# Kernel tuning notes

Hardware: AMD Instinct MI355X
Metric: run time of the kernel (lower is better)

Reference implementation:

```python
import jax, jax.numpy as jnp
import numpy as np

T, B, D, H = 1024, 4, 1024, 16
HD = D // H  # 64


def _layernorm(x, g, b, eps=1e-5):
    mu = jnp.mean(x, axis=-1, keepdims=True)
    var = jnp.var(x, axis=-1, keepdims=True)
    return (x - mu) / jnp.sqrt(var + eps) * g + b


def setup_inputs() -> dict:
    key = jax.random.key(0)
    ks = jax.random.split(key, 16)
    s = 1.0 / np.sqrt(D)
    mk = lambda k: jax.random.uniform(k, (D, D), jnp.float32, -s, s)
    return {
        "x": jax.random.normal(ks[0], (T, B, D), jnp.float32),
        "Wq": mk(ks[1]), "bq": jnp.zeros((D,), jnp.float32),
        "Wk": mk(ks[2]), "bk": jnp.zeros((D,), jnp.float32),
        "Wv": mk(ks[3]), "bv": jnp.zeros((D,), jnp.float32),
        "Wo": mk(ks[4]), "bo": jnp.zeros((D,), jnp.float32),
        "Wl": mk(ks[5]), "bl": jnp.zeros((D,), jnp.float32),
        "g1": jnp.ones((D,), jnp.float32), "b1": jnp.zeros((D,), jnp.float32),
        "g2": jnp.ones((D,), jnp.float32), "b2": jnp.zeros((D,), jnp.float32),
    }


def reference(x, Wq, bq, Wk, bk, Wv, bv, Wo, bo, Wl, bl, g1, b1, g2, b2):
    # x: [T, B, D] (time-major). The torch loop over dim 0 with full keys/values
    # is equivalent to batched full (non-causal) self-attention.
    q = (x @ Wq.T + bq).reshape(T, B, H, HD)
    k = (x @ Wk.T + bk).reshape(T, B, H, HD)
    v = (x @ Wv.T + bv).reshape(T, B, H, HD)
    scores = jnp.einsum("tbhd,sbhd->bhts", q, k) / np.sqrt(HD).astype(np.float32)
    attn = jax.nn.softmax(scores, axis=-1)          # [B,H,T,T]
    ctx = jnp.einsum("bhts,sbhd->tbhd", attn, v).reshape(T, B, D)
    attn_out = ctx @ Wo.T + bo
    # dropout p: identity at inference
    h = _layernorm(attn_out + x, g1, b1)
    ffn = h @ Wl.T + bl
    return _layernorm(ffn + h, g2, b2)
```

## Files before the change

kernel.cpp:

```cpp
#include <hip/hip_runtime.h>

#define T_ 1024
#define B_ 4
#define D_ 1024
#define H_ 16
#define HD_ 64
#define M_ (T_ * B_)

typedef _Float16 f16;
typedef f16 f16x8 __attribute__((ext_vector_type(8)));
typedef f16 f16x4 __attribute__((ext_vector_type(4)));
typedef float f32x4 __attribute__((ext_vector_type(4)));

__device__ __forceinline__ void gl2lds16(const void* g, void* l) {
  __builtin_amdgcn_global_load_lds(
      (const __attribute__((address_space(1))) void*)g,
      (__attribute__((address_space(3))) void*)l, 16, 0, 0);
}

__global__ __launch_bounds__(256) void cvt_f32_f16(const float* __restrict__ in,
                                                   f16* __restrict__ out, int n) {
  int i = (blockIdx.x * 256 + threadIdx.x) * 4;
  if (i >= n) return;
  float4 v = *(const float4*)(in + i);
  f16x4 o = {(f16)v.x, (f16)v.y, (f16)v.z, (f16)v.w};
  *(f16x4*)(out + i) = o;
}

struct WPtrs {
  const float* s[5];
  f16* d[5];
};

__global__ __launch_bounds__(256) void cvt5(WPtrs p) {
  const int a = blockIdx.x >> 10;
  const int i = ((blockIdx.x & 1023) * 256 + threadIdx.x) * 4;
  float4 v = *(const float4*)(p.s[a] + i);
  f16x4 o = {(f16)v.x, (f16)v.y, (f16)v.z, (f16)v.w};
  *(f16x4*)(p.d[a] + i) = o;
}

__global__ __launch_bounds__(256) void bcat(const float* __restrict__ b0,
                                            const float* __restrict__ b1,
                                            const float* __restrict__ b2,
                                            float* __restrict__ dst) {
  const float* src = blockIdx.x == 0 ? b0 : (blockIdx.x == 1 ? b1 : b2);
  const int i = threadIdx.x * 4;
  *(float4*)(dst + blockIdx.x * 1024 + i) = *(const float4*)(src + i);
}

__global__ __launch_bounds__(256) void gemm_f16(const f16* __restrict__ A,
                                                const f16* __restrict__ W,
                                                const float* __restrict__ bias,
                                                float* __restrict__ out) {
  constexpr int K = D_, BK = 32;
  __shared__ __align__(16) f16 As[128 * BK];
  __shared__ __align__(16) f16 Bs[64 * BK];
  const int tid = threadIdx.x;
  const int lane = tid & 63;
  const int quad = lane >> 4, l16 = lane & 15;
  const int m0 = blockIdx.y * 128, n0 = blockIdx.x * 64;
  const int wave = tid >> 6;
  const int wm = (wave >> 1) * 64, wn = (wave & 1) * 32;
  f32x4 acc[4][2] = {};
  for (int kt = 0; kt < K / BK; ++kt) {
    __syncthreads();
    const int kb = kt * BK;
#pragma unroll
    for (int i = 0; i < 2; ++i) {
      const int c = i * 256 + tid;
      const int row = c >> 2, col8 = (c & 3) * 8;
      const int ldsbase = (i * 256 + (tid & ~63)) * 8;
      gl2lds16(A + (size_t)(m0 + row) * K + kb + col8, &As[ldsbase]);
    }
    {
      const int row = tid >> 2, col8 = (tid & 3) * 8;
      const int ldsbase = (tid & ~63) * 8;
      gl2lds16(W + (size_t)(n0 + row) * K + kb + col8, &Bs[ldsbase]);
    }
    __syncthreads();
    f16x8 af[4], bf[2];
#pragma unroll
    for (int i = 0; i < 4; ++i)
      af[i] = *(const f16x8*)&As[(wm + i * 16 + l16) * BK + quad * 8];
#pragma unroll
    for (int j = 0; j < 2; ++j)
      bf[j] = *(const f16x8*)&Bs[(wn + j * 16 + l16) * BK + quad * 8];
#pragma unroll
    for (int i = 0; i < 4; ++i)
#pragma unroll
      for (int j = 0; j < 2; ++j)
        acc[i][j] = __builtin_amdgcn_mfma_f32_16x16x32_f16(af[i], bf[j], acc[i][j], 0, 0, 0);
  }
#pragma unroll
  for (int j = 0; j < 2; ++j) {
    const int n = n0 + wn + j * 16 + l16;
    const float bn = bias[n];
#pragma unroll
    for (int i = 0; i < 4; ++i) {
      const int m = m0 + wm + i * 16 + quad * 4;
#pragma unroll
      for (int r = 0; r < 4; ++r)
        out[(size_t)(m + r) * D_ + n] = acc[i][j][r] + bn;
    }
  }
}

#define QSCALE 0.18033688011112042f
__global__ __launch_bounds__(256) void gemm_qkv(const f16* __restrict__ A,
                                                const f16* __restrict__ W,
                                                const float* __restrict__ bias,
                                                f16* __restrict__ qo,
                                                f16* __restrict__ ko,
                                                f16* __restrict__ vo) {
  constexpr int K = D_, BK = 32;
  __shared__ __align__(16) f16 As[128 * BK];
  __shared__ __align__(16) f16 Bs[128 * BK];
  const int tid = threadIdx.x;
  const int lane = tid & 63;
  const int quad = lane >> 4, l16 = lane & 15;
  const int m0 = blockIdx.y * 128, n0 = blockIdx.x * 128;
  const int wave = tid >> 6;
  const int wm = (wave >> 1) * 64, wn = (wave & 1) * 64;
  f32x4 acc[4][4] = {};
  for (int kt = 0; kt < K / BK; ++kt) {
    __syncthreads();
    const int kb = kt * BK;
#pragma unroll
    for (int i = 0; i < 2; ++i) {
      const int c = i * 256 + tid;
      const int row = c >> 2, col8 = (c & 3) * 8;
      const int ldsbase = (i * 256 + (tid & ~63)) * 8;
      gl2lds16(A + (size_t)(m0 + row) * K + kb + col8, &As[ldsbase]);
      gl2lds16(W + (size_t)(n0 + row) * K + kb + col8, &Bs[ldsbase]);
    }
    __syncthreads();
    f16x8 af[4], bf[4];
#pragma unroll
    for (int i = 0; i < 4; ++i)
      af[i] = *(const f16x8*)&As[(wm + i * 16 + l16) * BK + quad * 8];
#pragma unroll
    for (int j = 0; j < 4; ++j)
      bf[j] = *(const f16x8*)&Bs[(wn + j * 16 + l16) * BK + quad * 8];
#pragma unroll
    for (int i = 0; i < 4; ++i)
#pragma unroll
      for (int j = 0; j < 4; ++j)
        acc[i][j] = __builtin_amdgcn_mfma_f32_16x16x32_f16(af[i], bf[j], acc[i][j], 0, 0, 0);
  }
  const int which = n0 >> 10;
  f16* outp = which == 0 ? qo : (which == 1 ? ko : vo);
  const float sc = which == 0 ? QSCALE : 1.0f;
#pragma unroll
  for (int j = 0; j < 4; ++j) {
    const int n = n0 + wn + j * 16 + l16;
    const float bn = bias[n];
    const int nl = n & 1023;
    const int hh = nl >> 6, d = nl & 63;
#pragma unroll
    for (int i = 0; i < 4; ++i) {
#pragma unroll
      for (int r = 0; r < 4; ++r) {
        const int m = m0 + wm + i * 16 + quad * 4 + r;
        const float v = (acc[i][j][r] + bn) * sc;
        const int t = m >> 2, bb = m & 3;
        if (which < 2)
          outp[((size_t)(bb * H_ + hh) * T_ + t) * HD_ + d] = (f16)v;
        else
          outp[((size_t)(bb * H_ + hh) * HD_ + d) * T_ + t] = (f16)v;
      }
    }
  }
}

__global__ __launch_bounds__(256) void attn(const f16* __restrict__ Q,
                                            const f16* __restrict__ Km,
                                            const f16* __restrict__ Vt,
                                            f16* __restrict__ ctx) {
  constexpr int SK = 128;
  constexpr int NT = T_ / SK;
  __shared__ __align__(16) f16 Ks[SK * HD_];
  __shared__ __align__(16) f16 Vs[HD_ * SK];
  __shared__ __align__(16) f16 Ps[4][16 * 36];
  const int tid = threadIdx.x, wave = tid >> 6, lane = tid & 63;
  const int quad = lane >> 4, l16 = lane & 15;
  const int b = blockIdx.z, h = blockIdx.y, q0 = blockIdx.x * 64;
  const f16* Qbh = Q + ((size_t)(b * H_ + h) * T_ + q0 + wave * 16) * HD_;
  const f16* Kbh = Km + (size_t)(b * H_ + h) * T_ * HD_;
  const f16* Vbh = Vt + (size_t)(b * H_ + h) * HD_ * T_;

  const f16x8 qf0 = *(const f16x8*)&Qbh[l16 * HD_ + quad * 8];
  const f16x8 qf1 = *(const f16x8*)&Qbh[l16 * HD_ + 32 + quad * 8];

  f32x4 O[4] = {};
  float l = 0.f;
  const int sw = l16 & 7;

  for (int kt = 0; kt < NT; ++kt) {
    const int s0 = kt * SK;
    __syncthreads();
#pragma unroll
    for (int it = 0; it < 4; ++it) {
      const int n = wave * 256 + it * 64 + lane;
      const int s = n >> 3, cp = n & 7, cl = cp ^ (s & 7);
      gl2lds16(Kbh + (size_t)(s0 + s) * HD_ + cl * 8, &Ks[(wave * 256 + it * 64) * 8]);
    }
#pragma unroll
    for (int it = 0; it < 4; ++it) {
      const int n = wave * 256 + it * 64 + lane;
      const int d = n >> 4, cp = n & 15, cl = cp ^ (d & 7);
      gl2lds16(Vbh + (size_t)d * T_ + s0 + cl * 8, &Vs[(wave * 256 + it * 64) * 8]);
    }
    __syncthreads();

    float st[8][4];
#pragma unroll
    for (int s = 0; s < 8; ++s) {
      const int row = s * 16 + l16;
      const f16x8 ka = *(const f16x8*)&Ks[row * HD_ + (quad ^ sw) * 8];
      const f16x8 kb = *(const f16x8*)&Ks[row * HD_ + ((4 + quad) ^ sw) * 8];
      f32x4 a = {};
      a = __builtin_amdgcn_mfma_f32_16x16x32_f16(ka, qf0, a, 0, 0, 0);
      a = __builtin_amdgcn_mfma_f32_16x16x32_f16(kb, qf1, a, 0, 0, 0);
#pragma unroll
      for (int r = 0; r < 4; ++r) {
        st[s][r] = exp2f(a[r]);
        l += st[s][r];
      }
    }

#pragma unroll
    for (int cI = 0; cI < 4; ++cI) {
      f16* pw = &Ps[wave][0];
      f16x4 w0, w1;
#pragma unroll
      for (int r = 0; r < 4; ++r) {
        w0[r] = (f16)st[2 * cI][r];
        w1[r] = (f16)st[2 * cI + 1][r];
      }
      *(f16x4*)&pw[l16 * 36 + quad * 4] = w0;
      *(f16x4*)&pw[l16 * 36 + 16 + quad * 4] = w1;
      const f16x8 pf = *(const f16x8*)&pw[l16 * 36 + quad * 8];
#pragma unroll
      for (int dt = 0; dt < 4; ++dt) {
        const int d = dt * 16 + l16;
        const f16x8 vf = *(const f16x8*)&Vs[d * SK + (((cI * 4 + quad) ^ sw) * 8)];
        O[dt] = __builtin_amdgcn_mfma_f32_16x16x32_f16(vf, pf, O[dt], 0, 0, 0);
      }
    }
  }

  l += __shfl_xor(l, 16, 64);
  l += __shfl_xor(l, 32, 64);
  const float linv = 1.f / l;
  const int t = q0 + wave * 16 + l16;
#pragma unroll
  for (int dt = 0; dt < 4; ++dt) {
    f16x4 ov;
#pragma unroll
    for (int r = 0; r < 4; ++r) ov[r] = (f16)(O[dt][r] * linv);
    *(f16x4*)&ctx[((size_t)t * B_ + b) * D_ + h * HD_ + dt * 16 + quad * 4] = ov;
  }
}

__global__ __launch_bounds__(256) void add_ln(const float* __restrict__ a,
                                              const float* __restrict__ res,
                                              const float* __restrict__ g,
                                              const float* __restrict__ bb,
                                              float* __restrict__ out,
                                              f16* __restrict__ outh) {
  const int row = blockIdx.x, tid = threadIdx.x;
  const size_t base = (size_t)row * D_;
  float4 va = *(const float4*)&a[base + tid * 4];
  float4 vr = *(const float4*)&res[base + tid * 4];
  float x0 = va.x + vr.x, x1 = va.y + vr.y, x2 = va.z + vr.z, x3 = va.w + vr.w;
  float s = x0 + x1 + x2 + x3;
  float sq = x0 * x0 + x1 * x1 + x2 * x2 + x3 * x3;
#pragma unroll
  for (int off = 32; off; off >>= 1) {
    s += __shfl_down(s, off, 64);
    sq += __shfl_down(sq, off, 64);
  }
  __shared__ float rs[4], rq[4];
  __shared__ float mean_s, rstd_s;
  if ((tid & 63) == 0) { rs[tid >> 6] = s; rq[tid >> 6] = sq; }
  __syncthreads();
  if (tid == 0) {
    float S = rs[0] + rs[1] + rs[2] + rs[3];
    float Qq = rq[0] + rq[1] + rq[2] + rq[3];
    float mean = S / D_;
    float var = Qq / D_ - mean * mean;
    mean_s = mean;
    rstd_s = rsqrtf(var + 1e-5f);
  }
  __syncthreads();
  const float mean = mean_s, rstd = rstd_s;
  float4 vg = *(const float4*)&g[tid * 4];
  float4 vb = *(const float4*)&bb[tid * 4];
  float y0 = (x0 - mean) * rstd * vg.x + vb.x;
  float y1 = (x1 - mean) * rstd * vg.y + vb.y;
  float y2 = (x2 - mean) * rstd * vg.z + vb.z;
  float y3 = (x3 - mean) * rstd * vg.w + vb.w;
  *(float4*)&out[base + tid * 4] = make_float4(y0, y1, y2, y3);
  if (outh) {
    f16x4 o = {(f16)y0, (f16)y1, (f16)y2, (f16)y3};
    *(f16x4*)&outh[base + tid * 4] = o;
  }
}

extern "C" void kernel_launch(void* const* d_in, const int* in_sizes, int n_in,
                              void* d_out, int out_size, void* d_ws, size_t ws_size,
                              hipStream_t stream) {
  const float* x  = (const float*)d_in[0];
  const float* Wq = (const float*)d_in[1];
  const float* bq = (const float*)d_in[2];
  const float* Wk = (const float*)d_in[3];
  const float* bk = (const float*)d_in[4];
  const float* Wv = (const float*)d_in[5];
  const float* bv = (const float*)d_in[6];
  const float* Wo = (const float*)d_in[7];
  const float* bo = (const float*)d_in[8];
  const float* Wl = (const float*)d_in[9];
  const float* bl = (const float*)d_in[10];
  const float* g1 = (const float*)d_in[11];
  const float* b1 = (const float*)d_in[12];
  const float* g2 = (const float*)d_in[13];
  const float* b2 = (const float*)d_in[14];

  char* ws = (char*)d_ws;
  const size_t MB = 1 << 20;
  f16*   xb   = (f16*)(ws + 0 * MB);
  f16*   wqkv = (f16*)(ws + 8 * MB);
  f16*   wob  = (f16*)(ws + 14 * MB);
  f16*   wlb  = (f16*)(ws + 16 * MB);
  float* bqkv = (float*)(ws + 18 * MB);
  f16*   qb   = (f16*)(ws + 19 * MB);
  f16*   kb   = (f16*)(ws + 27 * MB);
  f16*   vb   = (f16*)(ws + 35 * MB);
  f16*   ctxb = xb;
  float* att  = (float*)qb;
  f16*   hb   = vb;
  float* hbuf = (float*)ws;

  cvt_f32_f16<<<M_ * D_ / 1024, 256, 0, stream>>>(x, xb, M_ * D_);
  WPtrs wp;
  wp.s[0] = Wq; wp.s[1] = Wk; wp.s[2] = Wv; wp.s[3] = Wo; wp.s[4] = Wl;
  wp.d[0] = wqkv; wp.d[1] = wqkv + D_ * D_; wp.d[2] = wqkv + 2 * D_ * D_;
  wp.d[3] = wob; wp.d[4] = wlb;
  cvt5<<<5 * 1024, 256, 0, stream>>>(wp);
  bcat<<<3, 256, 0, stream>>>(bq, bk, bv, bqkv);

  gemm_qkv<<<dim3(3 * D_ / 128, M_ / 128), 256, 0, stream>>>(xb, wqkv, bqkv, qb, kb, vb);

  attn<<<dim3(T_ / 64, H_, B_), 256, 0, stream>>>(qb, kb, vb, ctxb);

  dim3 gg(D_ / 64, M_ / 128);
  gemm_f16<<<gg, 256, 0, stream>>>(ctxb, wob, bo, att);
  add_ln<<<M_, 256, 0, stream>>>(att, x, g1, b1, hbuf, hb);
  gemm_f16<<<gg, 256, 0, stream>>>(hb, wlb, bl, att);
  add_ln<<<M_, 256, 0, stream>>>(att, hbuf, g2, b2, (float*)d_out, nullptr);
}
```

Baseline: 254.3 us.

## Double query rows per attention wave and fuse residual add into GEMM epilogue

The attention kernel now has each wave handle 32 query rows instead of 16. Each K/V tile loaded into LDS is reused across twice as many queries, and the grid is halved. The K/V global pointers are precomputed and advanced incrementally instead of recomputed every iteration. The residual add moves from the layernorm kernel into the output GEMM epilogue, so add_ln becomes a plain layernorm reading one tensor. In exchange, attention register pressure rises and fewer blocks launch, while the GEMM epilogue gains a strided residual read.

Result: no change. 255.0 us (+0.3%).

```diff
diff --git a/kernel.cpp b/kernel.cpp
--- a/kernel.cpp
+++ b/kernel.cpp
@@ -52,6 +52,7 @@
 __global__ __launch_bounds__(256) void gemm_f16(const f16* __restrict__ A,
                                                 const f16* __restrict__ W,
                                                 const float* __restrict__ bias,
+                                                const float* __restrict__ res,
                                                 float* __restrict__ out) {
   constexpr int K = D_, BK = 32;
   __shared__ __align__(16) f16 As[128 * BK];
@@ -101,7 +102,7 @@
       const int m = m0 + wm + i * 16 + quad * 4;
 #pragma unroll
       for (int r = 0; r < 4; ++r)
-        out[(size_t)(m + r) * D_ + n] = acc[i][j][r] + bn;
+        out[(size_t)(m + r) * D_ + n] = acc[i][j][r] + bn + res[(size_t)(m + r) * D_ + n];
     }
   }
 }
@@ -184,96 +185,118 @@
   __shared__ __align__(16) f16 Ps[4][16 * 36];
   const int tid = threadIdx.x, wave = tid >> 6, lane = tid & 63;
   const int quad = lane >> 4, l16 = lane & 15;
-  const int b = blockIdx.z, h = blockIdx.y, q0 = blockIdx.x * 64;
-  const f16* Qbh = Q + ((size_t)(b * H_ + h) * T_ + q0 + wave * 16) * HD_;
+  const int b = blockIdx.z, h = blockIdx.y, q0 = blockIdx.x * 128;
+  const f16* Qbh = Q + ((size_t)(b * H_ + h) * T_ + q0 + wave * 32) * HD_;
   const f16* Kbh = Km + (size_t)(b * H_ + h) * T_ * HD_;
   const f16* Vbh = Vt + (size_t)(b * H_ + h) * HD_ * T_;
 
-  const f16x8 qf0 = *(const f16x8*)&Qbh[l16 * HD_ + quad * 8];
-  const f16x8 qf1 = *(const f16x8*)&Qbh[l16 * HD_ + 32 + quad * 8];
-
-  f32x4 O[4] = {};
-  float l = 0.f;
+  f16x8 qf[2][2];
+#pragma unroll
+  for (int c = 0; c < 2; ++c) {
+    qf[c][0] = *(const f16x8*)&Qbh[(c * 16 + l16) * HD_ + quad * 8];
+    qf[c][1] = *(const f16x8*)&Qbh[(c * 16 + l16) * HD_ + 32 + quad * 8];
+  }
+
+  const f16* kq[4];
+  const f16* vq[4];
+  int lds_o[4];
+#pragma unroll
+  for (int it = 0; it < 4; ++it) {
+    const int n = wave * 256 + it * 64 + lane;
+    const int s = n >> 3, cp = n & 7, cl = cp ^ (s & 7);
+    kq[it] = Kbh + (size_t)s * HD_ + cl * 8;
+    const int d = n >> 4, cp2 = n & 15, cl2 = cp2 ^ (d & 7);
+    vq[it] = Vbh + (size_t)d * T_ + cl2 * 8;
+    lds_o[it] = (wave * 256 + it * 64) * 8;
+  }
+
+  f32x4 O[4][2] = {};
+  float lsum[2] = {0.f, 0.f};
   const int sw = l16 & 7;
 
   for (int kt = 0; kt < NT; ++kt) {
-    const int s0 = kt * SK;
     __syncthreads();
 #pragma unroll
     for (int it = 0; it < 4; ++it) {
-      const int n = wave * 256 + it * 64 + lane;
-      const int s = n >> 3, cp = n & 7, cl = cp ^ (s & 7);
-      gl2lds16(Kbh + (size_t)(s0 + s) * HD_ + cl * 8, &Ks[(wave * 256 + it * 64) * 8]);
+      gl2lds16(kq[it], &Ks[lds_o[it]]);
+      kq[it] += SK * HD_;
     }
 #pragma unroll
     for (int it = 0; it < 4; ++it) {
-      const int n = wave * 256 + it * 64 + lane;
-      const int d = n >> 4, cp = n & 15, cl = cp ^ (d & 7);
-      gl2lds16(Vbh + (size_t)d * T_ + s0 + cl * 8, &Vs[(wave * 256 + it * 64) * 8]);
-    }
-    __syncthreads();
-
-    float st[8][4];
+      gl2lds16(vq[it], &Vs[lds_o[it]]);
+      vq[it] += SK;
+    }
+    __syncthreads();
+
+    float st[8][2][4];
 #pragma unroll
     for (int s = 0; s < 8; ++s) {
       const int row = s * 16 + l16;
       const f16x8 ka = *(const f16x8*)&Ks[row * HD_ + (quad ^ sw) * 8];
       const f16x8 kb = *(const f16x8*)&Ks[row * HD_ + ((4 + quad) ^ sw) * 8];
-      f32x4 a = {};
-      a = __builtin_amdgcn_mfma_f32_16x16x32_f16(ka, qf0, a, 0, 0, 0);
-      a = __builtin_amdgcn_mfma_f32_16x16x32_f16(kb, qf1, a, 0, 0, 0);
-#pragma unroll
-      for (int r = 0; r < 4; ++r) {
-        st[s][r] = exp2f(a[r]);
-        l += st[s][r];
+#pragma unroll
+      for (int c = 0; c < 2; ++c) {
+        f32x4 a = {};
+        a = __builtin_amdgcn_mfma_f32_16x16x32_f16(ka, qf[c][0], a, 0, 0, 0);
+        a = __builtin_amdgcn_mfma_f32_16x16x32_f16(kb, qf[c][1], a, 0, 0, 0);
+#pragma unroll
+        for (int r = 0; r < 4; ++r) {
+          st[s][c][r] = exp2f(a[r]);
+          lsum[c] += st[s][c][r];
+        }
       }
     }
 
 #pragma unroll
     for (int cI = 0; cI < 4; ++cI) {
-      f16* pw = &Ps[wave][0];
-      f16x4 w0, w1;
-#pragma unroll
-      for (int r = 0; r < 4; ++r) {
-        w0[r] = (f16)st[2 * cI][r];
-        w1[r] = (f16)st[2 * cI + 1][r];
+#pragma unroll
+      for (int c = 0; c < 2; ++c) {
+        f16* pw = &Ps[wave][0];
+        f16x4 w0, w1;
+#pragma unroll
+        for (int r = 0; r < 4; ++r) {
+          w0[r] = (f16)st[2 * cI][c][r];
+          w1[r] = (f16)st[2 * cI + 1][c][r];
+        }
+        *(f16x4*)&pw[l16 * 36 + quad * 4] = w0;
+        *(f16x4*)&pw[l16 * 36 + 16 + quad * 4] = w1;
+        const f16x8 pf = *(const f16x8*)&pw[l16 * 36 + quad * 8];
+#pragma unroll
+        for (int dt = 0; dt < 4; ++dt) {
+          const int d = dt * 16 + l16;
+          const f16x8 vf = *(const f16x8*)&Vs[d * SK + (((cI * 4 + quad) ^ sw) * 8)];
+          O[dt][c] = __builtin_amdgcn_mfma_f32_16x16x32_f16(vf, pf, O[dt][c], 0, 0, 0);
+        }
       }
-      *(f16x4*)&pw[l16 * 36 + quad * 4] = w0;
-      *(f16x4*)&pw[l16 * 36 + 16 + quad * 4] = w1;
-      const f16x8 pf = *(const f16x8*)&pw[l16 * 36 + quad * 8];
-#pragma unroll
-      for (int dt = 0; dt < 4; ++dt) {
-        const int d = dt * 16 + l16;
-        const f16x8 vf = *(const f16x8*)&Vs[d * SK + (((cI * 4 + quad) ^ sw) * 8)];
-        O[dt] = __builtin_amdgcn_mfma_f32_16x16x32_f16(vf, pf, O[dt], 0, 0, 0);
-      }
-    }
-  }
-
-  l += __shfl_xor(l, 16, 64);
-  l += __shfl_xor(l, 32, 64);
-  const float linv = 1.f / l;
-  const int t = q0 + wave * 16 + l16;
-#pragma unroll
-  for (int dt = 0; dt < 4; ++dt) {
-    f16x4 ov;
-#pragma unroll
-    for (int r = 0; r < 4; ++r) ov[r] = (f16)(O[dt][r] * linv);
-    *(f16x4*)&ctx[((size_t)t * B_ + b) * D_ + h * HD_ + dt * 16 + quad * 4] = ov;
-  }
-}
-
-__global__ __launch_bounds__(256) void add_ln(const float* __restrict__ a,
-                                              const float* __restrict__ res,
-                                              const float* __restrict__ g,
-                                              const float* __restrict__ bb,
-                                              float* __restrict__ out,
-                                              f16* __restrict__ outh) {
+    }
+  }
+
+#pragma unroll
+  for (int c = 0; c < 2; ++c) {
+    float l = lsum[c];
+    l += __shfl_xor(l, 16, 64);
+    l += __shfl_xor(l, 32, 64);
+    const float linv = 1.f / l;
+    const int t = q0 + wave * 32 + c * 16 + l16;
+#pragma unroll
+    for (int dt = 0; dt < 4; ++dt) {
+      f16x4 ov;
+#pragma unroll
+      for (int r = 0; r < 4; ++r) ov[r] = (f16)(O[dt][c][r] * linv);
+      *(f16x4*)&ctx[((size_t)t * B_ + b) * D_ + h * HD_ + dt * 16 + quad * 4] = ov;
+    }
+  }
+}
+
+__global__ __launch_bounds__(256) void lnorm(const float* __restrict__ a,
+                                             const float* __restrict__ g,
+                                             const float* __restrict__ bb,
+                                             float* __restrict__ out,
+                                             f16* __restrict__ outh) {
   const int row = blockIdx.x, tid = threadIdx.x;
   const size_t base = (size_t)row * D_;
   float4 va = *(const float4*)&a[base + tid * 4];
-  float4 vr = *(const float4*)&res[base + tid * 4];
-  float x0 = va.x + vr.x, x1 = va.y + vr.y, x2 = va.z + vr.z, x3 = va.w + vr.w;
+  float x0 = va.x, x1 = va.y, x2 = va.z, x3 = va.w;
   float s = x0 + x1 + x2 + x3;
   float sq = x0 * x0 + x1 * x1 + x2 * x2 + x3 * x3;
 #pragma unroll
@@ -352,11 +375,11 @@
 
   gemm_qkv<<<dim3(3 * D_ / 128, M_ / 128), 256, 0, stream>>>(xb, wqkv, bqkv, qb, kb, vb);
 
-  attn<<<dim3(T_ / 64, H_, B_), 256, 0, stream>>>(qb, kb, vb, ctxb);
+  attn<<<dim3(T_ / 128, H_, B_), 256, 0, stream>>>(qb, kb, vb, ctxb);
 
   dim3 gg(D_ / 64, M_ / 128);
-  gemm_f16<<<gg, 256, 0, stream>>>(ctxb, wob, bo, att);
-  add_ln<<<M_, 256, 0, stream>>>(att, x, g1, b1, hbuf, hb);
-  gemm_f16<<<gg, 256, 0, stream>>>(hb, wlb, bl, att);
-  add_ln<<<M_, 256, 0, stream>>>(att, hbuf, g2, b2, (float*)d_out, nullptr);
-}
+  gemm_f16<<<gg, 256, 0, stream>>>(ctxb, wob, bo, x, att);
+  lnorm<<<M_, 256, 0, stream>>>(att, g1, b1, hbuf, hb);
+  gemm_f16<<<gg, 256, 0, stream>>>(hb, wlb, bl, hbuf, att);
+  lnorm<<<M_, 256, 0, stream>>>(att, g2, b2, (float*)d_out, nullptr);
+}
```
